# Performance work log

Measured on AMD Instinct MI355X. Metric: run time of the kernel, lower is better.

The kernel has to match this reference:

```python
import jax, jax.numpy as jnp
import numpy as np
import math

B, S, H = 4, 2048, 1024


def setup_inputs() -> dict:
    key = jax.random.key(0)
    ks = jax.random.split(key, 9)
    scale = 1.0 / math.sqrt(H)
    x = jax.random.normal(ks[0], (B, S, H), dtype=jnp.float32)
    attention_mask = jax.random.randint(ks[1], (B, S, S), 0, 2, dtype=jnp.int32)
    Wq = jax.random.uniform(ks[2], (H, H), jnp.float32, -scale, scale)
    bq = jax.random.uniform(ks[3], (H,), jnp.float32, -scale, scale)
    Wk = jax.random.uniform(ks[4], (H, H), jnp.float32, -scale, scale)
    bk = jax.random.uniform(ks[5], (H,), jnp.float32, -scale, scale)
    Wv = jax.random.uniform(ks[6], (H, H), jnp.float32, -scale, scale)
    bv = jax.random.uniform(ks[7], (H,), jnp.float32, -scale, scale)
    return {"x": x, "attention_mask": attention_mask,
            "Wq": Wq, "bq": bq, "Wk": Wk, "bk": bk, "Wv": Wv, "bv": bv}


def reference(x, attention_mask, Wq, bq, Wk, bk, Wv, bv):
    # q/k/v projections (torch Linear: x @ W.T + b)
    q = jnp.einsum('bsh,oh->bso', x, Wq) + bq
    k = jnp.einsum('bsh,oh->bso', x, Wk) + bk
    v = jnp.einsum('bsh,oh->bso', x, Wv) + bv
    # raw scores [B,S,S]
    scores = jnp.einsum('bqh,bkh->bqk', q, k)
    # NOTE: faithful to original - mask fill happens BEFORE the 1/sqrt(H) scaling
    scores = jnp.where(attention_mask == 0, jnp.float32(-1e9), scores)
    attn = jax.nn.softmax(scores / math.sqrt(H), axis=-1)
    # dropout p=0.0 (eval mode) -> identity
    return jnp.einsum('bqk,bkh->bqh', attn, v)
```

## Files before the change

kernel.cpp:

```cpp
#include <hip/hip_runtime.h>

#define B_ 4
#define S_ 2048
#define H_ 1024

typedef __bf16 bf16x8 __attribute__((ext_vector_type(8)));
typedef float  f32x4  __attribute__((ext_vector_type(4)));

__device__ __forceinline__ unsigned short f2bf(float f) {
  unsigned u = __float_as_uint(f);
  u += 0x7FFF + ((u >> 16) & 1);
  return (unsigned short)(u >> 16);
}

__global__ void cvt_all_kernel(const float* __restrict__ x,
                               const float* __restrict__ wq,
                               const float* __restrict__ wk,
                               const float* __restrict__ wv,
                               unsigned short* __restrict__ dst) {
  int i = blockIdx.x * blockDim.x + threadIdx.x;
  const int NX = (B_ * S_ * H_) / 4;
  const int NW = (H_ * H_) / 4;
  const float* src; int off;
  if (i < NX) { src = x; off = i; }
  else { int j = i - NX; int w = j >> 18; off = j & (NW - 1);
         src = (w == 0) ? wq : (w == 1) ? wk : wv; }
  float4 v = reinterpret_cast<const float4*>(src)[off];
  ushort4 o; o.x = f2bf(v.x); o.y = f2bf(v.y); o.z = f2bf(v.z); o.w = f2bf(v.w);
  reinterpret_cast<ushort4*>(dst)[i] = o;
}


__device__ __forceinline__ bf16x8 lfrag(const char* base, int row, int kb) {
  return *reinterpret_cast<const bf16x8*>(base + row * 128 + (kb ^ ((row & 7) << 4)));
}

__device__ __forceinline__ void stage_q(const unsigned short* __restrict__ g,
                                        long row0, long ld, int k0e,
                                        char* sbase, int q, int t) {
  int row = q * 64 + (t >> 3);
  int osw = ((t & 7) << 4) ^ ((row & 7) << 4);
  const char* gp = reinterpret_cast<const char*>(g + (row0 + row) * ld + k0e) + osw;
  char* lp = sbase + q * 8192 + ((t >> 6) << 10);
  __builtin_amdgcn_global_load_lds((const __attribute__((address_space(1))) void*)gp,
                                   (__attribute__((address_space(3))) void*)lp,
                                   16, 0, 0);
}

template <int NT>
__device__ __forceinline__ void gemm8(const unsigned short* __restrict__ A, long ldA, long m0,
                                      const unsigned short* __restrict__ Bm, long ldB, long n0,
                                      char* sm, f32x4 acc[8][4]) {
  const int t = threadIdx.x;
  const int lane = t & 63;
  const int wid = t >> 6;
  const int wr = wid >> 2, wc = wid & 3;
  const int lrow = lane & 15;
  const int kb0 = (lane >> 4) * 16;
  char* sA0 = sm;          char* sB0 = sm + 32768;
  char* sA1 = sm + 65536;  char* sB1 = sm + 98304;

#pragma unroll
  for (int q = 0; q < 4; ++q) stage_q(A, m0, ldA, 0, sA0, q, t);
#pragma unroll
  for (int q = 0; q < 4; ++q) stage_q(Bm, n0, ldB, 0, sB0, q, t);
#pragma unroll
  for (int q = 0; q < 4; ++q) stage_q(Bm, n0, ldB, 64, sB1, q, t);
  stage_q(A, m0, ldA, 64, sA1, 0, t);
  stage_q(A, m0, ldA, 64, sA1, 2, t);
  asm volatile("s_waitcnt vmcnt(6)" ::: "memory");
  __builtin_amdgcn_s_barrier();

  auto ktile = [&](int kt, char* cA, char* cB, char* nA) {
    const int k1 = (kt + 1 < NT ? kt + 1 : NT - 1) * 64;
    const int k2 = (kt + 2 < NT ? kt + 2 : NT - 1) * 64;
    bf16x8 bfr[4][2], af[2][2];
#pragma unroll
    for (int nf = 0; nf < 4; ++nf)
#pragma unroll
      for (int ks = 0; ks < 2; ++ks)
        bfr[nf][ks] = lfrag(cB, wc * 64 + nf * 16 + lrow, ks * 64 + kb0);
#pragma unroll
    for (int mf = 0; mf < 2; ++mf)
#pragma unroll
      for (int ks = 0; ks < 2; ++ks)
        af[mf][ks] = lfrag(cA, wr * 128 + mf * 16 + lrow, ks * 64 + kb0);
    stage_q(A, m0, ldA, k1, nA, 1, t);
    stage_q(A, m0, ldA, k1, nA, 3, t);
    __builtin_amdgcn_s_barrier();
    asm volatile("s_waitcnt lgkmcnt(0)" ::: "memory");
    __builtin_amdgcn_sched_barrier(0);
    __builtin_amdgcn_s_setprio(1);
#pragma unroll
    for (int mf = 0; mf < 2; ++mf)
#pragma unroll
      for (int nf = 0; nf < 4; ++nf)
#pragma unroll
        for (int ks = 0; ks < 2; ++ks)
          acc[mf][nf] = __builtin_amdgcn_mfma_f32_16x16x32_bf16(af[mf][ks], bfr[nf][ks], acc[mf][nf], 0, 0, 0);
    __builtin_amdgcn_s_setprio(0);
    __builtin_amdgcn_s_barrier();
#pragma unroll
    for (int q = 1; q < 4; ++q) {
#pragma unroll
      for (int mf = 0; mf < 2; ++mf)
#pragma unroll
        for (int ks = 0; ks < 2; ++ks)
          af[mf][ks] = lfrag(cA, wr * 128 + q * 32 + mf * 16 + lrow, ks * 64 + kb0);
      if (q == 1) { stage_q(Bm, n0, ldB, k2, cB, 0, t); stage_q(Bm, n0, ldB, k2, cB, 1, t); }
      if (q == 2) { stage_q(Bm, n0, ldB, k2, cB, 2, t); stage_q(Bm, n0, ldB, k2, cB, 3, t); }
      if (q == 3) { stage_q(A, m0, ldA, k2, cA, 0, t); stage_q(A, m0, ldA, k2, cA, 2, t);
                    asm volatile("s_waitcnt vmcnt(6)" ::: "memory"); }
      __builtin_amdgcn_s_barrier();
      asm volatile("s_waitcnt lgkmcnt(0)" ::: "memory");
      __builtin_amdgcn_sched_barrier(0);
      __builtin_amdgcn_s_setprio(1);
#pragma unroll
      for (int mf = 0; mf < 2; ++mf)
#pragma unroll
        for (int nf = 0; nf < 4; ++nf)
#pragma unroll
          for (int ks = 0; ks < 2; ++ks)
            acc[2 * q + mf][nf] = __builtin_amdgcn_mfma_f32_16x16x32_bf16(af[mf][ks], bfr[nf][ks], acc[2 * q + mf][nf], 0, 0, 0);
      __builtin_amdgcn_s_setprio(0);
      __builtin_amdgcn_s_barrier();
    }
  };

#pragma unroll 1
  for (int kt = 0; kt < NT; kt += 2) {
    ktile(kt,     sA0, sB0, sA1);
    ktile(kt + 1, sA1, sB1, sA0);
  }
}

__global__ __launch_bounds__(512, 2) void qkv_kernel(
    const unsigned short* __restrict__ x, const unsigned short* __restrict__ W3,
    const float* __restrict__ bq, const float* __restrict__ bk, const float* __restrict__ bv,
    unsigned short* __restrict__ Q, unsigned short* __restrict__ K, unsigned short* __restrict__ V) {
  extern __shared__ char sm[];
  const int z = blockIdx.z;
  const unsigned short* W = W3 + (size_t)z * (H_ * H_);
  const float* bias = (z == 0) ? bq : (z == 1) ? bk : bv;
  unsigned short* out = (z == 0) ? Q : (z == 1) ? K : V;
  const long m0 = (long)blockIdx.y * 256, n0 = (long)blockIdx.x * 256;
  f32x4 acc[8][4] = {};
  gemm8<H_ / 64>(x, H_, m0, W, H_, n0, sm, acc);
  const int lane = threadIdx.x & 63;
  const int wid = threadIdx.x >> 6;
  const int wr = wid >> 2, wc = wid & 3;
#pragma unroll
  for (int nf = 0; nf < 4; ++nf) {
    long col = n0 + wc * 64 + nf * 16 + (lane & 15);
    float bb = bias[col];
#pragma unroll
    for (int mq = 0; mq < 8; ++mq)
#pragma unroll
      for (int r = 0; r < 4; ++r) {
        long row = m0 + wr * 128 + mq * 16 + (lane >> 4) * 4 + r;
        out[row * H_ + col] = f2bf(acc[mq][nf][r] + bb);
      }
  }
}

__global__ void vtrans_kernel(const unsigned short* __restrict__ V,
                              unsigned short* __restrict__ VT) {
  __shared__ unsigned short tile[64][66];
  const int b = blockIdx.z;
  const int c0 = blockIdx.x * 64;
  const int r0 = blockIdx.y * 64;
  const int tx = threadIdx.x, ty = threadIdx.y;
  const unsigned short* Vb = V + (size_t)b * S_ * H_;
  unsigned short* VTb = VT + (size_t)b * H_ * S_;
#pragma unroll
  for (int i = 0; i < 16; ++i) {
    int r = ty * 16 + i;
    tile[r][tx] = Vb[(size_t)(r0 + r) * H_ + c0 + tx];
  }
  __syncthreads();
#pragma unroll
  for (int i = 0; i < 16; ++i) {
    int c = ty * 16 + i;
    VTb[(size_t)(c0 + c) * S_ + r0 + tx] = tile[tx][c];
  }
}

__global__ __launch_bounds__(512, 2) void scores_kernel(
    const unsigned short* __restrict__ Q, const unsigned short* __restrict__ Km,
    const int* __restrict__ mask, unsigned short* __restrict__ P,
    float* __restrict__ rowsum) {
  extern __shared__ char sm[];
  const int b = blockIdx.z;
  const long m0 = (long)blockIdx.y * 256, n0 = (long)blockIdx.x * 256;
  const unsigned short* Qb = Q + (size_t)b * S_ * H_;
  const unsigned short* Kb = Km + (size_t)b * S_ * H_;
  const int* Mb = mask + (size_t)b * S_ * S_;
  unsigned short* Pb = P + (size_t)b * S_ * S_;
  f32x4 acc[8][4] = {};
  gemm8<H_ / 64>(Qb, H_, m0, Kb, H_, n0, sm, acc);
  const int lane = threadIdx.x & 63;
  const int wid = threadIdx.x >> 6;
  const int wr = wid >> 2, wc = wid & 3;
#pragma unroll
  for (int mq = 0; mq < 8; ++mq) {
#pragma unroll
    for (int r = 0; r < 4; ++r) {
      long row = m0 + wr * 128 + mq * 16 + (lane >> 4) * 4 + r;
      float rs = 0.f;
#pragma unroll
      for (int nf = 0; nf < 4; ++nf) {
        long col = n0 + wc * 64 + nf * 16 + (lane & 15);
        float p = Mb[row * S_ + col] ? __expf(acc[mq][nf][r] * 0.03125f) : 0.f;
        Pb[row * S_ + col] = f2bf(p);
        rs += p;
      }
#pragma unroll
      for (int s = 1; s < 16; s <<= 1) rs += __shfl_xor(rs, s, 64);
      if ((lane & 15) == 0) atomicAdd(&rowsum[(size_t)b * S_ + row], rs);
    }
  }
}

__global__ __launch_bounds__(512, 2) void pv_kernel(
    const unsigned short* __restrict__ P, const unsigned short* __restrict__ VT,
    const float* __restrict__ rowsum, float* __restrict__ out) {
  extern __shared__ char sm[];
  const int b = blockIdx.z;
  const long m0 = (long)blockIdx.y * 256, n0 = (long)blockIdx.x * 256;
  const unsigned short* Pb = P + (size_t)b * S_ * S_;
  const unsigned short* VTb = VT + (size_t)b * H_ * S_;
  f32x4 acc[8][4] = {};
  gemm8<S_ / 64>(Pb, S_, m0, VTb, S_, n0, sm, acc);
  const int lane = threadIdx.x & 63;
  const int wid = threadIdx.x >> 6;
  const int wr = wid >> 2, wc = wid & 3;
#pragma unroll
  for (int mq = 0; mq < 8; ++mq)
#pragma unroll
    for (int r = 0; r < 4; ++r) {
      long row = m0 + wr * 128 + mq * 16 + (lane >> 4) * 4 + r;
      float inv = 1.f / rowsum[(size_t)b * S_ + row];
#pragma unroll
      for (int nf = 0; nf < 4; ++nf) {
        long col = n0 + wc * 64 + nf * 16 + (lane & 15);
        out[((size_t)b * S_ + row) * H_ + col] = acc[mq][nf][r] * inv;
      }
    }
}

extern "C" void kernel_launch(void* const* d_in, const int* in_sizes, int n_in,
                              void* d_out, int out_size, void* d_ws, size_t ws_size,
                              hipStream_t stream) {
  const float* x   = (const float*)d_in[0];
  const int* mask  = (const int*)d_in[1];
  const float* Wq  = (const float*)d_in[2];
  const float* bq  = (const float*)d_in[3];
  const float* Wk  = (const float*)d_in[4];
  const float* bk  = (const float*)d_in[5];
  const float* Wv  = (const float*)d_in[6];
  const float* bv  = (const float*)d_in[7];
  float* out = (float*)d_out;

  const size_t MS = (size_t)B_ * S_ * H_;
  unsigned short* xb  = (unsigned short*)d_ws;
  unsigned short* W3  = xb + MS;
  unsigned short* Qb  = W3 + (size_t)3 * H_ * H_;
  unsigned short* Kb  = Qb + MS;
  unsigned short* Vb  = Kb + MS;
  unsigned short* VTb = Vb + MS;
  unsigned short* Pb  = VTb + MS;
  float* rowsum = (float*)(Pb + (size_t)B_ * S_ * S_);

  (void)hipFuncSetAttribute(reinterpret_cast<const void*>(qkv_kernel),
                            hipFuncAttributeMaxDynamicSharedMemorySize, 131072);
  (void)hipFuncSetAttribute(reinterpret_cast<const void*>(scores_kernel),
                            hipFuncAttributeMaxDynamicSharedMemorySize, 131072);
  (void)hipFuncSetAttribute(reinterpret_cast<const void*>(pv_kernel),
                            hipFuncAttributeMaxDynamicSharedMemorySize, 131072);

  hipMemsetAsync(rowsum, 0, (size_t)B_ * S_ * sizeof(float), stream);

  const int NCVT = (int)(MS / 4) + 3 * (H_ * H_ / 4);
  cvt_all_kernel<<<NCVT / 256, 256, 0, stream>>>(x, Wq, Wk, Wv, xb);

  qkv_kernel<<<dim3(H_ / 256, (B_ * S_) / 256, 3), 512, 131072, stream>>>(
      xb, W3, bq, bk, bv, Qb, Kb, Vb);

  vtrans_kernel<<<dim3(H_ / 64, S_ / 64, B_), dim3(64, 4), 0, stream>>>(Vb, VTb);

  scores_kernel<<<dim3(S_ / 256, S_ / 256, B_), 512, 131072, stream>>>(
      Qb, Kb, mask, Pb, rowsum);

  pv_kernel<<<dim3(H_ / 256, S_ / 256, B_), 512, 131072, stream>>>(Pb, VTb, rowsum, out);
}
```

Measured before the change: 324.3 us.

## Stage GEMM epilogues through LDS, bit-pack mask, fuse V transpose into QKV

The Q/K, scores and PV epilogues now stage accumulators through a padded per-wave LDS buffer so each lane writes contiguous 16-byte rows, replacing scattered 2- and 4-byte global stores. A separate pass packs the int32 attention mask into a bitmask with ballot, so the scores epilogue reads one byte per eight columns instead of the full int mask. The V projection writes its transpose directly with 4-element column stores, which removes the separate transpose kernel and the intermediate V buffer. The costs are the extra mask-pack launch, which still reads the full mask, and LDS round trips in every epilogue.

After: 320.1 us. About the same (-1.3%).

```diff
diff --git a/kernel.cpp b/kernel.cpp
--- a/kernel.cpp
+++ b/kernel.cpp
@@ -6,6 +6,7 @@
 
 typedef __bf16 bf16x8 __attribute__((ext_vector_type(8)));
 typedef float  f32x4  __attribute__((ext_vector_type(4)));
+typedef short  short8 __attribute__((ext_vector_type(8)));
 
 __device__ __forceinline__ unsigned short f2bf(float f) {
   unsigned u = __float_as_uint(f);
@@ -30,6 +31,18 @@
   reinterpret_cast<ushort4*>(dst)[i] = o;
 }
 
+__global__ void maskpack_kernel(const int* __restrict__ mask,
+                                unsigned long long* __restrict__ mpk) {
+  const int lane = threadIdx.x & 63;
+  const long row = (long)blockIdx.x * 4 + (threadIdx.x >> 6);
+  const int* mrow = mask + row * S_;
+#pragma unroll
+  for (int w = 0; w < S_ / 64; ++w) {
+    int v = mrow[w * 64 + lane];
+    unsigned long long b = __ballot(v != 0);
+    if (lane == 0) mpk[row * (S_ / 64) + w] = b;
+  }
+}
 
 __device__ __forceinline__ bf16x8 lfrag(const char* base, int row, int kb) {
   return *reinterpret_cast<const bf16x8*>(base + row * 128 + (kb ^ ((row & 7) << 4)));
@@ -134,89 +147,128 @@
   }
 }
 
+#define EPI_PITCH 68
+
 __global__ __launch_bounds__(512, 2) void qkv_kernel(
     const unsigned short* __restrict__ x, const unsigned short* __restrict__ W3,
     const float* __restrict__ bq, const float* __restrict__ bk, const float* __restrict__ bv,
-    unsigned short* __restrict__ Q, unsigned short* __restrict__ K, unsigned short* __restrict__ V) {
+    unsigned short* __restrict__ Q, unsigned short* __restrict__ K, unsigned short* __restrict__ VT) {
   extern __shared__ char sm[];
   const int z = blockIdx.z;
   const unsigned short* W = W3 + (size_t)z * (H_ * H_);
   const float* bias = (z == 0) ? bq : (z == 1) ? bk : bv;
-  unsigned short* out = (z == 0) ? Q : (z == 1) ? K : V;
   const long m0 = (long)blockIdx.y * 256, n0 = (long)blockIdx.x * 256;
   f32x4 acc[8][4] = {};
   gemm8<H_ / 64>(x, H_, m0, W, H_, n0, sm, acc);
+
   const int lane = threadIdx.x & 63;
   const int wid = threadIdx.x >> 6;
   const int wr = wid >> 2, wc = wid & 3;
-#pragma unroll
-  for (int nf = 0; nf < 4; ++nf) {
-    long col = n0 + wc * 64 + nf * 16 + (lane & 15);
-    float bb = bias[col];
+  const int g = lane >> 4, c = lane & 15;
+  float bb[4];
+#pragma unroll
+  for (int nf = 0; nf < 4; ++nf) bb[nf] = bias[n0 + wc * 64 + nf * 16 + c];
+
+  if (z == 2) {
 #pragma unroll
     for (int mq = 0; mq < 8; ++mq)
 #pragma unroll
-      for (int r = 0; r < 4; ++r) {
-        long row = m0 + wr * 128 + mq * 16 + (lane >> 4) * 4 + r;
-        out[row * H_ + col] = f2bf(acc[mq][nf][r] + bb);
+      for (int nf = 0; nf < 4; ++nf) {
+        long col = n0 + wc * 64 + nf * 16 + c;
+        long row0 = m0 + wr * 128 + mq * 16 + g * 4;
+        long bidx = row0 >> 11;
+        long srow = row0 & (S_ - 1);
+        ushort4 o;
+        o.x = f2bf(acc[mq][nf][0] + bb[nf]);
+        o.y = f2bf(acc[mq][nf][1] + bb[nf]);
+        o.z = f2bf(acc[mq][nf][2] + bb[nf]);
+        o.w = f2bf(acc[mq][nf][3] + bb[nf]);
+        *reinterpret_cast<ushort4*>(VT + bidx * H_ * S_ + col * S_ + srow) = o;
       }
-  }
-}
-
-__global__ void vtrans_kernel(const unsigned short* __restrict__ V,
-                              unsigned short* __restrict__ VT) {
-  __shared__ unsigned short tile[64][66];
-  const int b = blockIdx.z;
-  const int c0 = blockIdx.x * 64;
-  const int r0 = blockIdx.y * 64;
-  const int tx = threadIdx.x, ty = threadIdx.y;
-  const unsigned short* Vb = V + (size_t)b * S_ * H_;
-  unsigned short* VTb = VT + (size_t)b * H_ * S_;
-#pragma unroll
-  for (int i = 0; i < 16; ++i) {
-    int r = ty * 16 + i;
-    tile[r][tx] = Vb[(size_t)(r0 + r) * H_ + c0 + tx];
-  }
-  __syncthreads();
-#pragma unroll
-  for (int i = 0; i < 16; ++i) {
-    int c = ty * 16 + i;
-    VTb[(size_t)(c0 + c) * S_ + r0 + tx] = tile[tx][c];
+  } else {
+    unsigned short* out = (z == 0) ? Q : K;
+    float* wbuf = reinterpret_cast<float*>(sm) + wid * (32 * EPI_PITCH);
+#pragma unroll
+    for (int p = 0; p < 4; ++p) {
+#pragma unroll
+      for (int h2 = 0; h2 < 2; ++h2)
+#pragma unroll
+        for (int nf = 0; nf < 4; ++nf)
+#pragma unroll
+          for (int r = 0; r < 4; ++r)
+            wbuf[(h2 * 16 + g * 4 + r) * EPI_PITCH + nf * 16 + c] = acc[p * 2 + h2][nf][r] + bb[nf];
+      asm volatile("s_waitcnt lgkmcnt(0)" ::: "memory");
+      __builtin_amdgcn_sched_barrier(0);
+#pragma unroll
+      for (int it = 0; it < 4; ++it) {
+        int lr = it * 8 + (lane >> 3);
+        long row = m0 + wr * 128 + p * 32 + lr;
+        const float* src = wbuf + lr * EPI_PITCH + (lane & 7) * 8;
+        float4 v0 = *reinterpret_cast<const float4*>(src);
+        float4 v1 = *reinterpret_cast<const float4*>(src + 4);
+        short8 o;
+        o[0] = f2bf(v0.x); o[1] = f2bf(v0.y); o[2] = f2bf(v0.z); o[3] = f2bf(v0.w);
+        o[4] = f2bf(v1.x); o[5] = f2bf(v1.y); o[6] = f2bf(v1.z); o[7] = f2bf(v1.w);
+        *reinterpret_cast<short8*>(out + row * H_ + n0 + wc * 64 + (lane & 7) * 8) = o;
+      }
+    }
   }
 }
 
 __global__ __launch_bounds__(512, 2) void scores_kernel(
     const unsigned short* __restrict__ Q, const unsigned short* __restrict__ Km,
-    const int* __restrict__ mask, unsigned short* __restrict__ P,
+    const unsigned char* __restrict__ mpkb, unsigned short* __restrict__ P,
     float* __restrict__ rowsum) {
   extern __shared__ char sm[];
   const int b = blockIdx.z;
   const long m0 = (long)blockIdx.y * 256, n0 = (long)blockIdx.x * 256;
   const unsigned short* Qb = Q + (size_t)b * S_ * H_;
   const unsigned short* Kb = Km + (size_t)b * S_ * H_;
-  const int* Mb = mask + (size_t)b * S_ * S_;
+  const unsigned char* Mb = mpkb + (size_t)b * S_ * (S_ / 8);
   unsigned short* Pb = P + (size_t)b * S_ * S_;
   f32x4 acc[8][4] = {};
   gemm8<H_ / 64>(Qb, H_, m0, Kb, H_, n0, sm, acc);
+
   const int lane = threadIdx.x & 63;
   const int wid = threadIdx.x >> 6;
   const int wr = wid >> 2, wc = wid & 3;
-#pragma unroll
-  for (int mq = 0; mq < 8; ++mq) {
-#pragma unroll
-    for (int r = 0; r < 4; ++r) {
-      long row = m0 + wr * 128 + mq * 16 + (lane >> 4) * 4 + r;
+  const int g = lane >> 4, c = lane & 15;
+  float* wbuf = reinterpret_cast<float*>(sm) + wid * (32 * EPI_PITCH);
+#pragma unroll
+  for (int p = 0; p < 4; ++p) {
+#pragma unroll
+    for (int h2 = 0; h2 < 2; ++h2)
+#pragma unroll
+      for (int nf = 0; nf < 4; ++nf)
+#pragma unroll
+        for (int r = 0; r < 4; ++r)
+          wbuf[(h2 * 16 + g * 4 + r) * EPI_PITCH + nf * 16 + c] = acc[p * 2 + h2][nf][r];
+    asm volatile("s_waitcnt lgkmcnt(0)" ::: "memory");
+    __builtin_amdgcn_sched_barrier(0);
+#pragma unroll
+    for (int it = 0; it < 4; ++it) {
+      int lr = it * 8 + (lane >> 3);
+      long row = m0 + wr * 128 + p * 32 + lr;
+      const float* src = wbuf + lr * EPI_PITCH + (lane & 7) * 8;
+      float4 v0 = *reinterpret_cast<const float4*>(src);
+      float4 v1 = *reinterpret_cast<const float4*>(src + 4);
+      unsigned mb = Mb[row * (S_ / 8) + ((n0 + wc * 64) >> 3) + (lane & 7)];
+      float pv[8];
+      pv[0] = v0.x; pv[1] = v0.y; pv[2] = v0.z; pv[3] = v0.w;
+      pv[4] = v1.x; pv[5] = v1.y; pv[6] = v1.z; pv[7] = v1.w;
       float rs = 0.f;
-#pragma unroll
-      for (int nf = 0; nf < 4; ++nf) {
-        long col = n0 + wc * 64 + nf * 16 + (lane & 15);
-        float p = Mb[row * S_ + col] ? __expf(acc[mq][nf][r] * 0.03125f) : 0.f;
-        Pb[row * S_ + col] = f2bf(p);
-        rs += p;
+      short8 o;
+#pragma unroll
+      for (int j = 0; j < 8; ++j) {
+        float pj = ((mb >> j) & 1) ? __expf(pv[j] * 0.03125f) : 0.f;
+        rs += pj;
+        o[j] = (short)f2bf(pj);
       }
-#pragma unroll
-      for (int s = 1; s < 16; s <<= 1) rs += __shfl_xor(rs, s, 64);
-      if ((lane & 15) == 0) atomicAdd(&rowsum[(size_t)b * S_ + row], rs);
+      *reinterpret_cast<short8*>(Pb + row * S_ + n0 + wc * 64 + (lane & 7) * 8) = o;
+      rs += __shfl_xor(rs, 1, 64);
+      rs += __shfl_xor(rs, 2, 64);
+      rs += __shfl_xor(rs, 4, 64);
+      if ((lane & 7) == 0) atomicAdd(&rowsum[(size_t)b * S_ + row], rs);
     }
   }
 }
@@ -231,21 +283,34 @@
   const unsigned short* VTb = VT + (size_t)b * H_ * S_;
   f32x4 acc[8][4] = {};
   gemm8<S_ / 64>(Pb, S_, m0, VTb, S_, n0, sm, acc);
+
   const int lane = threadIdx.x & 63;
   const int wid = threadIdx.x >> 6;
   const int wr = wid >> 2, wc = wid & 3;
-#pragma unroll
-  for (int mq = 0; mq < 8; ++mq)
-#pragma unroll
-    for (int r = 0; r < 4; ++r) {
-      long row = m0 + wr * 128 + mq * 16 + (lane >> 4) * 4 + r;
-      float inv = 1.f / rowsum[(size_t)b * S_ + row];
-#pragma unroll
-      for (int nf = 0; nf < 4; ++nf) {
-        long col = n0 + wc * 64 + nf * 16 + (lane & 15);
-        out[((size_t)b * S_ + row) * H_ + col] = acc[mq][nf][r] * inv;
-      }
+  const int g = lane >> 4, c = lane & 15;
+  float* wbuf = reinterpret_cast<float*>(sm) + wid * (32 * EPI_PITCH);
+#pragma unroll
+  for (int p = 0; p < 4; ++p) {
+#pragma unroll
+    for (int h2 = 0; h2 < 2; ++h2)
+#pragma unroll
+      for (int nf = 0; nf < 4; ++nf)
+#pragma unroll
+        for (int r = 0; r < 4; ++r)
+          wbuf[(h2 * 16 + g * 4 + r) * EPI_PITCH + nf * 16 + c] = acc[p * 2 + h2][nf][r];
+    asm volatile("s_waitcnt lgkmcnt(0)" ::: "memory");
+    __builtin_amdgcn_sched_barrier(0);
+#pragma unroll
+    for (int it = 0; it < 8; ++it) {
+      int lr = it * 4 + (lane >> 4);
+      long row = m0 + wr * 128 + p * 32 + lr;
+      float inv = __frcp_rn(rowsum[(size_t)b * S_ + row]);
+      const float* src = wbuf + lr * EPI_PITCH + (lane & 15) * 4;
+      float4 v = *reinterpret_cast<const float4*>(src);
+      float4 o; o.x = v.x * inv; o.y = v.y * inv; o.z = v.z * inv; o.w = v.w * inv;
+      *reinterpret_cast<float4*>(out + ((size_t)b * S_ + row) * H_ + n0 + wc * 64 + (lane & 15) * 4) = o;
     }
+  }
 }
 
 extern "C" void kernel_launch(void* const* d_in, const int* in_sizes, int n_in,
@@ -266,10 +331,10 @@
   unsigned short* W3  = xb + MS;
   unsigned short* Qb  = W3 + (size_t)3 * H_ * H_;
   unsigned short* Kb  = Qb + MS;
-  unsigned short* Vb  = Kb + MS;
-  unsigned short* VTb = Vb + MS;
+  unsigned short* VTb = Kb + MS;
   unsigned short* Pb  = VTb + MS;
   float* rowsum = (float*)(Pb + (size_t)B_ * S_ * S_);
+  unsigned long long* mpk = (unsigned long long*)(rowsum + B_ * S_);
 
   (void)hipFuncSetAttribute(reinterpret_cast<const void*>(qkv_kernel),
                             hipFuncAttributeMaxDynamicSharedMemorySize, 131072);
@@ -283,13 +348,13 @@
   const int NCVT = (int)(MS / 4) + 3 * (H_ * H_ / 4);
   cvt_all_kernel<<<NCVT / 256, 256, 0, stream>>>(x, Wq, Wk, Wv, xb);
 
+  maskpack_kernel<<<(B_ * S_) / 4, 256, 0, stream>>>(mask, mpk);
+
   qkv_kernel<<<dim3(H_ / 256, (B_ * S_) / 256, 3), 512, 131072, stream>>>(
-      xb, W3, bq, bk, bv, Qb, Kb, Vb);
-
-  vtrans_kernel<<<dim3(H_ / 64, S_ / 64, B_), dim3(64, 4), 0, stream>>>(Vb, VTb);
+      xb, W3, bq, bk, bv, Qb, Kb, VTb);
 
   scores_kernel<<<dim3(S_ / 256, S_ / 256, B_), 512, 131072, stream>>>(
-      Qb, Kb, mask, Pb, rowsum);
+      Qb, Kb, (const unsigned char*)mpk, Pb, rowsum);
 
   pv_kernel<<<dim3(H_ / 256, S_ / 256, B_), 512, 131072, stream>>>(Pb, VTb, rowsum, out);
 }
```
